# Performance work log

Hardware: AMD Instinct MI355X
Metric: run time of the kernel (lower is better)

## Reference

```python
import jax, jax.numpy as jnp
import numpy as np

DIM, NH, NS = 384, 8, 3
HID = int(DIM * 4.0)
R1 = max(1, int(min(DIM, HID) * 0.5))   # 192
R2 = max(1, int(min(HID, DIM) * 0.5))   # 192
SPLIT = DIM // NS                        # 128
HD = DIM // NH                           # 48


def _ln(x, g, b, eps=1e-6):
    m = jnp.mean(x, axis=-1, keepdims=True)
    v = jnp.mean(jnp.square(x - m), axis=-1, keepdims=True)
    return (x - m) * jax.lax.rsqrt(v + eps) * g + b


def _dwconv(x, w, b):
    # x: [B, SPLIT, H, W]; w: [SPLIT, 1, 3, 3] depthwise (groups=SPLIT)
    y = jax.lax.conv_general_dilated(
        x, w, window_strides=(1, 1), padding='SAME',
        dimension_numbers=('NCHW', 'OIHW', 'NCHW'),
        feature_group_count=SPLIT)
    return y + b[None, :, None, None]


def setup_inputs() -> dict:
    key = jax.random.key(0)
    ks = jax.random.split(key, 16)
    s = lambda *sh: 0.02
    inp = {
        'x': jax.random.normal(ks[0], (16, DIM, 56, 56), jnp.float32),
        'dw_w0': jax.random.normal(ks[1], (SPLIT, 1, 3, 3), jnp.float32) * 0.1,
        'dw_b0': jnp.zeros((SPLIT,), jnp.float32),
        'dw_w1': jax.random.normal(ks[2], (SPLIT, 1, 3, 3), jnp.float32) * 0.1,
        'dw_b1': jnp.zeros((SPLIT,), jnp.float32),
        'ln1_g': jnp.ones((DIM,), jnp.float32),
        'ln1_b': jnp.zeros((DIM,), jnp.float32),
        'qkv_w': jax.random.normal(ks[3], (DIM, 3 * DIM), jnp.float32) * 0.02,
        'proj_w': jax.random.normal(ks[4], (DIM, DIM), jnp.float32) * 0.02,
        'proj_b': jnp.zeros((DIM,), jnp.float32),
        'ln2_g': jnp.ones((DIM,), jnp.float32),
        'ln2_b': jnp.zeros((DIM,), jnp.float32),
        'mlp1_dw': jax.random.normal(ks[5], (DIM, R1), jnp.float32) * 0.02,
        'mlp1_uw': jax.random.normal(ks[6], (R1, HID), jnp.float32) * 0.02,
        'mlp1_ub': jnp.zeros((HID,), jnp.float32),
        'mlp2_dw': jax.random.normal(ks[7], (HID, R2), jnp.float32) * 0.02,
        'mlp2_uw': jax.random.normal(ks[8], (R2, DIM), jnp.float32) * 0.02,
        'mlp2_ub': jnp.zeros((DIM,), jnp.float32),
    }
    return inp


def reference(x, dw_w0, dw_b0, dw_w1, dw_b1, ln1_g, ln1_b, qkv_w,
              proj_w, proj_b, ln2_g, ln2_b,
              mlp1_dw, mlp1_uw, mlp1_ub, mlp2_dw, mlp2_uw, mlp2_ub):
    B, C, H, W = x.shape
    # multi-scale depthwise residual chain
    s0, s1, s2 = jnp.split(x, NS, axis=1)
    s1 = _dwconv(s1 + s0, dw_w0, dw_b0)
    s2 = _dwconv(s2 + s1, dw_w1, dw_b1)
    x = jnp.concatenate([s0, s1, s2], axis=1)

    N = H * W
    x_flat = jnp.transpose(x.reshape(B, C, N), (0, 2, 1))  # [B, N, C]
    y = _ln(x_flat, ln1_g, ln1_b)
    qkv = (y @ qkv_w).reshape(B, N, 3, NH, HD)
    q = jnp.transpose(qkv[:, :, 0], (0, 2, 3, 1))  # [B, NH, HD, N]
    k = jnp.transpose(qkv[:, :, 1], (0, 2, 3, 1))
    v = jnp.transpose(qkv[:, :, 2], (0, 2, 3, 1))
    # L2 normalize over token dim (XCA)
    q = q / jnp.maximum(jnp.linalg.norm(q, axis=-1, keepdims=True), 1e-12)
    k = k / jnp.maximum(jnp.linalg.norm(k, axis=-1, keepdims=True), 1e-12)
    attn = jnp.einsum('bhdn,bhen->bhde', q, k)  # [B, NH, HD, HD]
    attn = jax.nn.softmax(attn, axis=-1)
    y = jnp.einsum('bhde,bhen->bhdn', attn, v)  # [B, NH, HD, N]
    y = jnp.transpose(y, (0, 3, 1, 2)).reshape(B, N, C)
    y = y @ proj_w + proj_b
    x_flat = x_flat + y

    z = _ln(x_flat, ln2_g, ln2_b)
    h = jax.nn.gelu((z @ mlp1_dw) @ mlp1_uw + mlp1_ub, approximate=False)
    z = (h @ mlp2_dw) @ mlp2_uw + mlp2_ub
    x_flat = x_flat + z
    return jnp.transpose(x_flat, (0, 2, 1)).reshape(B, C, H, W)
```

## Files before the change

kernel.cpp:

```cpp
#include <hip/hip_runtime.h>


typedef __attribute__((ext_vector_type(8))) short short8;
typedef __attribute__((ext_vector_type(4))) float floatx4;

#define NB 16
#define DIM 384
#define NTOK 3136
#define TTOK 50176
#define NH 8
#define HD 48

__device__ __forceinline__ unsigned short f2bf(float f) {
  union { float f; unsigned int u; } v; v.f = f;
  unsigned int u = v.u;
  unsigned int r = (u + 0x7FFFu + ((u >> 16) & 1u)) >> 16;
  return (unsigned short)r;
}
__device__ __forceinline__ float bf2f(unsigned short h) {
  union { unsigned int u; float f; } v; v.u = ((unsigned int)h) << 16;
  return v.f;
}

__device__ __forceinline__ void gload_lds16(const unsigned short* g, unsigned short* l) {
  __builtin_amdgcn_global_load_lds(
      (const __attribute__((address_space(1))) unsigned int*)g,
      (__attribute__((address_space(3))) unsigned int*)l, 16, 0, 0);
}

__global__ void zero_f32(float* __restrict__ p, int n) {
  int g = blockIdx.x * 256 + threadIdx.x;
  if (g < n) p[g] = 0.f;
}

__global__ void wtrans(const float* __restrict__ w, unsigned short* __restrict__ wt,
                       int K, int N) {
  int g = blockIdx.x * 256 + threadIdx.x;
  if (g < K * N) {
    int k = g / N, n = g % N;
    wt[(size_t)n * K + k] = f2bf(w[g]);
  }
}

__global__ void dwconv(const float* __restrict__ a, long bsA,
                       const float* __restrict__ b2, long bsB,
                       const float* __restrict__ w, const float* __restrict__ bias,
                       float* __restrict__ dst) {
  int g = blockIdx.x * 256 + threadIdx.x;
  int xx = g % 56;
  int yy = (g / 56) % 56;
  int c  = (g / NTOK) % 128;
  int b  = g / (NTOK * 128);
  const float* pa = a  + (size_t)b * bsA + (size_t)c * NTOK;
  const float* pb = b2 + (size_t)b * bsB + (size_t)c * NTOK;
  float acc = bias[c];
  #pragma unroll
  for (int ky = 0; ky < 3; ky++) {
    int y2 = yy + ky - 1;
    if (y2 < 0 || y2 >= 56) continue;
    #pragma unroll
    for (int kx = 0; kx < 3; kx++) {
      int x2 = xx + kx - 1;
      if (x2 < 0 || x2 >= 56) continue;
      acc += w[c * 9 + ky * 3 + kx] * (pa[y2 * 56 + x2] + pb[y2 * 56 + x2]);
    }
  }
  dst[((size_t)b * 128 + c) * NTOK + yy * 56 + xx] = acc;
}

__global__ __launch_bounds__(256) void build_ln1(
    const float* __restrict__ x, const float* __restrict__ s1,
    const float* __restrict__ s2, const float* __restrict__ g,
    const float* __restrict__ bb, float* __restrict__ xflat,
    unsigned short* __restrict__ y) {
  int tkn = blockIdx.x * 4 + (threadIdx.x >> 6);
  int lane = threadIdx.x & 63;
  int b = tkn / NTOK, n = tkn % NTOK;
  float v[6];
  float s = 0.f, sq = 0.f;
  #pragma unroll
  for (int i = 0; i < 6; i++) {
    int c = lane + i * 64;
    float t;
    if (c < 128)      t = x[((size_t)b * DIM + c) * NTOK + n];
    else if (c < 256) t = s1[((size_t)b * 128 + (c - 128)) * NTOK + n];
    else              t = s2[((size_t)b * 128 + (c - 256)) * NTOK + n];
    v[i] = t; s += t; sq += t * t;
  }
  #pragma unroll
  for (int off = 32; off; off >>= 1) {
    s += __shfl_xor(s, off);
    sq += __shfl_xor(sq, off);
  }
  float mean = s * (1.f / DIM);
  float var = sq * (1.f / DIM) - mean * mean;
  float rs = rsqrtf(var + 1e-6f);
  #pragma unroll
  for (int i = 0; i < 6; i++) {
    int c = lane + i * 64;
    size_t o = (size_t)tkn * DIM + c;
    xflat[o] = v[i];
    y[o] = f2bf((v[i] - mean) * rs * g[c] + bb[c]);
  }
}

__global__ __launch_bounds__(256) void ln_rows(
    const float* __restrict__ in, const float* __restrict__ g,
    const float* __restrict__ bb, unsigned short* __restrict__ out) {
  int tkn = blockIdx.x * 4 + (threadIdx.x >> 6);
  int lane = threadIdx.x & 63;
  const float* row = in + (size_t)tkn * DIM;
  float v[6];
  float s = 0.f, sq = 0.f;
  #pragma unroll
  for (int i = 0; i < 6; i++) {
    int c = lane + i * 64;
    v[i] = row[c]; s += v[i]; sq += v[i] * v[i];
  }
  #pragma unroll
  for (int off = 32; off; off >>= 1) {
    s += __shfl_xor(s, off);
    sq += __shfl_xor(sq, off);
  }
  float mean = s * (1.f / DIM);
  float var = sq * (1.f / DIM) - mean * mean;
  float rs = rsqrtf(var + 1e-6f);
  #pragma unroll
  for (int i = 0; i < 6; i++) {
    int c = lane + i * 64;
    out[(size_t)tkn * DIM + c] = f2bf((v[i] - mean) * rs * g[c] + bb[c]);
  }
}

template<int BN, int MODE>
__global__ __launch_bounds__(256) void gemm128(
    const unsigned short* __restrict__ A, const unsigned short* __restrict__ Bt,
    const float* __restrict__ bias, const float* __restrict__ resid,
    void* __restrict__ out, int M, int N, int K) {
  constexpr int MT = (BN == 128) ? 4 : 2;
  constexpr int NT = 4;
  __shared__ __align__(16) unsigned short As[128 * 32];
  __shared__ __align__(16) unsigned short Bs[BN * 32];
  const int tid = threadIdx.x;
  const int w = tid >> 6, lane = tid & 63;
  const int quad = lane >> 4, r16 = lane & 15;
  const int row0 = blockIdx.y * 128, col0 = blockIdx.x * BN;
  const int wm = (BN == 128) ? (w >> 1) * 64 : w * 32;
  const int wn = (BN == 128) ? (w & 1) * 64 : 0;
  const int lrow = lane >> 2;
  const int lcol = (lane & 3) * 8;

  const unsigned short* aP0 = A + (size_t)(row0 + w * 32 + lrow) * K + lcol;
  const unsigned short* aP1 = aP0 + (size_t)16 * K;
  const unsigned short* bP0 = Bt + (size_t)(col0 + ((BN == 128) ? w * 32 : w * 16) + lrow) * K + lcol;
  const unsigned short* bP1 = bP0 + (size_t)16 * K;

  floatx4 acc[MT][NT] = {};

  for (int k0 = 0; k0 < K; k0 += 32) {
    gload_lds16(aP0 + k0, &As[(2 * w) * 512]);
    gload_lds16(aP1 + k0, &As[(2 * w + 1) * 512]);
    if (BN == 128) {
      gload_lds16(bP0 + k0, &Bs[(2 * w) * 512]);
      gload_lds16(bP1 + k0, &Bs[(2 * w + 1) * 512]);
    } else {
      gload_lds16(bP0 + k0, &Bs[w * 512]);
    }
    __syncthreads();
    short8 af[MT], bfr[NT];
    #pragma unroll
    for (int mi = 0; mi < MT; mi++)
      af[mi] = *(const short8*)(&As[(wm + mi * 16 + r16) * 32 + quad * 8]);
    #pragma unroll
    for (int ni = 0; ni < NT; ni++)
      bfr[ni] = *(const short8*)(&Bs[(wn + ni * 16 + r16) * 32 + quad * 8]);
    #pragma unroll
    for (int mi = 0; mi < MT; mi++)
      #pragma unroll
      for (int ni = 0; ni < NT; ni++)
        acc[mi][ni] = __builtin_amdgcn_mfma_f32_16x16x32_bf16(af[mi], bfr[ni], acc[mi][ni], 0, 0, 0);
    __syncthreads();
  }

  #pragma unroll
  for (int mi = 0; mi < MT; mi++)
    #pragma unroll
    for (int ni = 0; ni < NT; ni++)
      #pragma unroll
      for (int p = 0; p < 4; p++) {
        int row = row0 + wm + mi * 16 + quad * 4 + p;
        int col = col0 + wn + ni * 16 + r16;
        size_t idx = (size_t)row * N + col;
        float v = acc[mi][ni][p];
        if (MODE == 0) {
          ((unsigned short*)out)[idx] = f2bf(v);
        } else if (MODE == 1) {
          v += bias[col];
          v = 0.5f * v * (1.0f + erff(v * 0.70710678118654752f));
          ((unsigned short*)out)[idx] = f2bf(v);
        } else {
          v += bias[col] + resid[idx];
          ((float*)out)[idx] = v;
        }
      }
}

__global__ __launch_bounds__(256) void attn_partial(
    const unsigned short* __restrict__ qkv, float* __restrict__ S,
    float* __restrict__ sq) {
  __shared__ float qs[64][48];
  __shared__ float ks[64][48];
  int blk = blockIdx.x;
  int b = blk / 392, rem = blk % 392;
  int h = rem / 49, chunk = rem % 49;
  int t = threadIdx.x;
  #pragma unroll
  for (int i = 0; i < 12; i++) {
    int idx = t + i * 256;
    int r = idx / 48, d = idx % 48;
    size_t ro = ((size_t)b * NTOK + chunk * 64 + r) * 1152 + h * HD;
    qs[r][d] = bf2f(qkv[ro + d]);
    ks[r][d] = bf2f(qkv[ro + 384 + d]);
  }
  __syncthreads();
  int d0 = (t >> 4) * 3, e0 = (t & 15) * 3;
  float acc[3][3] = {};
  #pragma unroll 4
  for (int r = 0; r < 64; r++) {
    float q0 = qs[r][d0], q1 = qs[r][d0 + 1], q2 = qs[r][d0 + 2];
    float k0 = ks[r][e0], k1 = ks[r][e0 + 1], k2 = ks[r][e0 + 2];
    acc[0][0] += q0 * k0; acc[0][1] += q0 * k1; acc[0][2] += q0 * k2;
    acc[1][0] += q1 * k0; acc[1][1] += q1 * k1; acc[1][2] += q1 * k2;
    acc[2][0] += q2 * k0; acc[2][1] += q2 * k1; acc[2][2] += q2 * k2;
  }
  float* Sp = S + (size_t)(b * NH + h) * 2304;
  #pragma unroll
  for (int i = 0; i < 3; i++)
    #pragma unroll
    for (int j = 0; j < 3; j++)
      atomicAdd(&Sp[(d0 + i) * 48 + e0 + j], acc[i][j]);
  if (t < 48) {
    float s = 0.f;
    for (int r = 0; r < 64; r++) s += qs[r][t] * qs[r][t];
    atomicAdd(&sq[b * 768 + h * HD + t], s);
  } else if (t >= 64 && t < 112) {
    int e = t - 64;
    float s = 0.f;
    for (int r = 0; r < 64; r++) s += ks[r][e] * ks[r][e];
    atomicAdd(&sq[b * 768 + 384 + h * HD + e], s);
  }
}

__global__ __launch_bounds__(64) void attn_softmax(
    float* __restrict__ S, const float* __restrict__ sq) {
  int bh = blockIdx.x, b = bh >> 3, h = bh & 7;
  int t = threadIdx.x;
  if (t >= 48) return;
  float qn = fmaxf(sqrtf(sq[b * 768 + h * HD + t]), 1e-12f);
  float* Sp = S + (size_t)bh * 2304 + t * 48;
  float row[48];
  float m = -1e30f;
  for (int e = 0; e < 48; e++) {
    float kn = fmaxf(sqrtf(sq[b * 768 + 384 + h * HD + e]), 1e-12f);
    row[e] = Sp[e] / (qn * kn);
    m = fmaxf(m, row[e]);
  }
  float ssum = 0.f;
  for (int e = 0; e < 48; e++) { row[e] = expf(row[e] - m); ssum += row[e]; }
  float inv = 1.f / ssum;
  for (int e = 0; e < 48; e++) Sp[e] = row[e] * inv;
}

__global__ __launch_bounds__(256) void attn_apply(
    const unsigned short* __restrict__ qkv, const float* __restrict__ attnb,
    unsigned short* __restrict__ yat) {
  __shared__ float att[48][48];
  int bh = blockIdx.x / 13, chunk = blockIdx.x % 13;
  int b = bh >> 3, h = bh & 7;
  int t = threadIdx.x;
  #pragma unroll
  for (int i = 0; i < 9; i++) {
    int idx = t + i * 256;
    if (idx < 2304) ((float*)att)[idx] = attnb[(size_t)bh * 2304 + idx];
  }
  __syncthreads();
  int n = chunk * 256 + t;
  if (n < NTOK) {
    float v[48];
    size_t ro = ((size_t)b * NTOK + n) * 1152 + 768 + h * HD;
    #pragma unroll
    for (int e = 0; e < 48; e++) v[e] = bf2f(qkv[ro + e]);
    size_t wo = ((size_t)b * NTOK + n) * DIM + h * HD;
    #pragma unroll 4
    for (int d = 0; d < 48; d++) {
      float s = 0.f;
      #pragma unroll
      for (int e = 0; e < 48; e++) s += att[d][e] * v[e];
      yat[wo + d] = f2bf(s);
    }
  }
}

__global__ __launch_bounds__(256) void transpose_out(const float* __restrict__ in,
                                                     float* __restrict__ out) {
  __shared__ float tile[32][33];
  int b = blockIdx.z, ct = blockIdx.y, nt = blockIdx.x;
  int t = threadIdx.x;
  int cc = t & 31, rr = t >> 5;
  #pragma unroll
  for (int i = 0; i < 4; i++) {
    int nn = rr + i * 8;
    tile[nn][cc] = in[((size_t)b * NTOK + nt * 32 + nn) * DIM + ct * 32 + cc];
  }
  __syncthreads();
  #pragma unroll
  for (int i = 0; i < 4; i++) {
    int c2 = rr + i * 8;
    out[((size_t)b * DIM + ct * 32 + c2) * NTOK + nt * 32 + cc] = tile[cc][c2];
  }
}

extern "C" void kernel_launch(void* const* d_in, const int* in_sizes, int n_in,
                              void* d_out, int out_size, void* d_ws, size_t ws_size,
                              hipStream_t stream) {
  const float* x       = (const float*)d_in[0];
  const float* dw_w0   = (const float*)d_in[1];
  const float* dw_b0   = (const float*)d_in[2];
  const float* dw_w1   = (const float*)d_in[3];
  const float* dw_b1   = (const float*)d_in[4];
  const float* ln1_g   = (const float*)d_in[5];
  const float* ln1_b   = (const float*)d_in[6];
  const float* qkv_w   = (const float*)d_in[7];
  const float* proj_w  = (const float*)d_in[8];
  const float* proj_b  = (const float*)d_in[9];
  const float* ln2_g   = (const float*)d_in[10];
  const float* ln2_b   = (const float*)d_in[11];
  const float* mlp1_dw = (const float*)d_in[12];
  const float* mlp1_uw = (const float*)d_in[13];
  const float* mlp1_ub = (const float*)d_in[14];
  const float* mlp2_dw = (const float*)d_in[15];
  const float* mlp2_uw = (const float*)d_in[16];
  const float* mlp2_ub = (const float*)d_in[17];
  float* out = (float*)d_out;
  char* ws = (char*)d_ws;

  float*          xflat = (float*)(ws + 0);
  unsigned short* qkvb  = (unsigned short*)(ws + 77070336);
  float*          s1ws  = (float*)(ws + 77070336);
  float*          s2ws  = (float*)(ws + 102760448);
  unsigned short* ybf   = (unsigned short*)(ws + 192675840);
  unsigned short* yat   = (unsigned short*)(ws + 192675840);
  float*          xres  = (float*)(ws + 77070336);
  unsigned short* zbf   = (unsigned short*)(ws + 0);
  unsigned short* h1    = (unsigned short*)(ws + 38535168);
  unsigned short* h3    = (unsigned short*)(ws + 57802752);
  unsigned short* h2    = (unsigned short*)(ws + 154140672);
  unsigned short* qkvT  = (unsigned short*)(ws + 231211008);
  unsigned short* projT = (unsigned short*)(ws + 232095744);
  unsigned short* m1dT  = (unsigned short*)(ws + 232390656);
  unsigned short* m1uT  = (unsigned short*)(ws + 232538112);
  unsigned short* m2dT  = (unsigned short*)(ws + 233127936);
  unsigned short* m2uT  = (unsigned short*)(ws + 233717760);
  float*          sqbuf = (float*)(ws + 233865216);
  float*          attnb = (float*)(ws + 233914368);

  zero_f32<<<1200, 256, 0, stream>>>(sqbuf, 307200);

  wtrans<<<1728, 256, 0, stream>>>(qkv_w, qkvT, 384, 1152);
  wtrans<<<576, 256, 0, stream>>>(proj_w, projT, 384, 384);
  wtrans<<<288, 256, 0, stream>>>(mlp1_dw, m1dT, 384, 192);
  wtrans<<<1152, 256, 0, stream>>>(mlp1_uw, m1uT, 192, 1536);
  wtrans<<<1152, 256, 0, stream>>>(mlp2_dw, m2dT, 1536, 192);
  wtrans<<<288, 256, 0, stream>>>(mlp2_uw, m2uT, 192, 384);

  dwconv<<<25088, 256, 0, stream>>>(x + 128 * NTOK, (long)DIM * NTOK,
                                    x, (long)DIM * NTOK, dw_w0, dw_b0, s1ws);
  dwconv<<<25088, 256, 0, stream>>>(x + 256 * NTOK, (long)DIM * NTOK,
                                    s1ws, (long)128 * NTOK, dw_w1, dw_b1, s2ws);

  build_ln1<<<12544, 256, 0, stream>>>(x, s1ws, s2ws, ln1_g, ln1_b, xflat, ybf);

  gemm128<128, 0><<<dim3(9, 392), 256, 0, stream>>>(ybf, qkvT, nullptr, nullptr,
                                                    qkvb, TTOK, 1152, 384);
  attn_partial<<<NB * NH * 49, 256, 0, stream>>>(qkvb, attnb, sqbuf);
  attn_softmax<<<NB * NH, 64, 0, stream>>>(attnb, sqbuf);
  attn_apply<<<NB * NH * 13, 256, 0, stream>>>(qkvb, attnb, yat);

  gemm128<128, 2><<<dim3(3, 392), 256, 0, stream>>>(yat, projT, proj_b, xflat,
                                                    xres, TTOK, 384, 384);
  ln_rows<<<12544, 256, 0, stream>>>(xres, ln2_g, ln2_b, zbf);
  gemm128<64, 0><<<dim3(3, 392), 256, 0, stream>>>(zbf, m1dT, nullptr, nullptr,
                                                   h1, TTOK, 192, 384);
  for (int half = 0; half < 2; half++) {
    const unsigned short* h1p = h1 + (size_t)half * 25088 * 192;
    unsigned short* h3p = h3 + (size_t)half * 25088 * 192;
    gemm128<128, 1><<<dim3(12, 196), 256, 0, stream>>>(h1p, m1uT, mlp1_ub, nullptr,
                                                       h2, 25088, 1536, 192);
    gemm128<64, 0><<<dim3(3, 196), 256, 0, stream>>>(h2, m2dT, nullptr, nullptr,
                                                     h3p, 25088, 192, 1536);
  }
  gemm128<128, 2><<<dim3(3, 392), 256, 0, stream>>>(h3, m2uT, mlp2_ub, xres,
                                                    xres, TTOK, 384, 192);
  transpose_out<<<dim3(98, 12, 16), 256, 0, stream>>>(xres, out);
}
```

Before: 992.2 us.

## Restructure LN1 transpose, attention reduction, and attention apply kernels

Result: faster. 885.8 us (-10.7%).

```diff
diff --git a/kernel.cpp b/kernel.cpp
--- a/kernel.cpp
+++ b/kernel.cpp
@@ -26,11 +26,6 @@
   __builtin_amdgcn_global_load_lds(
       (const __attribute__((address_space(1))) unsigned int*)g,
       (__attribute__((address_space(3))) unsigned int*)l, 16, 0, 0);
-}
-
-__global__ void zero_f32(float* __restrict__ p, int n) {
-  int g = blockIdx.x * 256 + threadIdx.x;
-  if (g < n) p[g] = 0.f;
 }
 
 __global__ void wtrans(const float* __restrict__ w, unsigned short* __restrict__ wt,
@@ -73,34 +68,55 @@
     const float* __restrict__ s2, const float* __restrict__ g,
     const float* __restrict__ bb, float* __restrict__ xflat,
     unsigned short* __restrict__ y) {
-  int tkn = blockIdx.x * 4 + (threadIdx.x >> 6);
-  int lane = threadIdx.x & 63;
-  int b = tkn / NTOK, n = tkn % NTOK;
-  float v[6];
-  float s = 0.f, sq = 0.f;
-  #pragma unroll
-  for (int i = 0; i < 6; i++) {
-    int c = lane + i * 64;
-    float t;
-    if (c < 128)      t = x[((size_t)b * DIM + c) * NTOK + n];
-    else if (c < 256) t = s1[((size_t)b * 128 + (c - 128)) * NTOK + n];
-    else              t = s2[((size_t)b * 128 + (c - 256)) * NTOK + n];
-    v[i] = t; s += t; sq += t * t;
-  }
-  #pragma unroll
-  for (int off = 32; off; off >>= 1) {
-    s += __shfl_xor(s, off);
-    sq += __shfl_xor(sq, off);
-  }
-  float mean = s * (1.f / DIM);
-  float var = sq * (1.f / DIM) - mean * mean;
-  float rs = rsqrtf(var + 1e-6f);
-  #pragma unroll
-  for (int i = 0; i < 6; i++) {
-    int c = lane + i * 64;
-    size_t o = (size_t)tkn * DIM + c;
-    xflat[o] = v[i];
-    y[o] = f2bf((v[i] - mean) * rs * g[c] + bb[c]);
+  __shared__ float tile[384 * 33];
+  __shared__ float psum[8][32], psumsq[8][32];
+  __shared__ float smean[32], srs[32];
+  int blk = blockIdx.x;
+  int b = blk / 98, n0 = (blk % 98) * 32;
+  int t = threadIdx.x;
+  int nl = t & 31, crow = t >> 5;
+
+  #pragma unroll 4
+  for (int i = 0; i < 48; i++) {
+    int c = i * 8 + crow;
+    float v;
+    if (c < 128)      v = x[((size_t)b * DIM + c) * NTOK + n0 + nl];
+    else if (c < 256) v = s1[((size_t)b * 128 + (c - 128)) * NTOK + n0 + nl];
+    else              v = s2[((size_t)b * 128 + (c - 256)) * NTOK + n0 + nl];
+    tile[c * 33 + nl] = v;
+  }
+  __syncthreads();
+
+  {
+    int seg = t >> 5, tok = t & 31;
+    float s = 0.f, sq = 0.f;
+    #pragma unroll 8
+    for (int cc = 0; cc < 48; cc++) {
+      float v = tile[(seg * 48 + cc) * 33 + tok];
+      s += v; sq += v * v;
+    }
+    psum[seg][tok] = s; psumsq[seg][tok] = sq;
+  }
+  __syncthreads();
+  if (t < 32) {
+    float s = 0.f, sq = 0.f;
+    #pragma unroll
+    for (int seg = 0; seg < 8; seg++) { s += psum[seg][t]; sq += psumsq[seg][t]; }
+    float mean = s * (1.f / DIM);
+    float var = sq * (1.f / DIM) - mean * mean;
+    smean[t] = mean;
+    srs[t] = rsqrtf(var + 1e-6f);
+  }
+  __syncthreads();
+
+  #pragma unroll 4
+  for (int i = 0; i < 48; i++) {
+    int idx = i * 256 + t;
+    int tok = idx / 384, c = idx - tok * 384;
+    float v = tile[c * 33 + tok];
+    size_t o = (size_t)(b * NTOK + n0 + tok) * DIM + c;
+    xflat[o] = v;
+    y[o] = f2bf((v - smean[tok]) * srs[tok] * g[c] + bb[c]);
   }
 }
 
@@ -206,99 +222,156 @@
 }
 
 __global__ __launch_bounds__(256) void attn_partial(
-    const unsigned short* __restrict__ qkv, float* __restrict__ S,
-    float* __restrict__ sq) {
-  __shared__ float qs[64][48];
-  __shared__ float ks[64][48];
+    const unsigned short* __restrict__ qkv, float* __restrict__ S_part,
+    float* __restrict__ sq_part) {
+  __shared__ float qs[48 * 68];
+  __shared__ float ks[48 * 68];
   int blk = blockIdx.x;
-  int b = blk / 392, rem = blk % 392;
-  int h = rem / 49, chunk = rem % 49;
+  int b = blk / 56, rem = blk % 56;
+  int h = rem / 7, chunk = rem % 7;
   int t = threadIdx.x;
-  #pragma unroll
-  for (int i = 0; i < 12; i++) {
-    int idx = t + i * 256;
-    int r = idx / 48, d = idx % 48;
-    size_t ro = ((size_t)b * NTOK + chunk * 64 + r) * 1152 + h * HD;
-    qs[r][d] = bf2f(qkv[ro + d]);
-    ks[r][d] = bf2f(qkv[ro + 384 + d]);
-  }
-  __syncthreads();
   int d0 = (t >> 4) * 3, e0 = (t & 15) * 3;
-  float acc[3][3] = {};
-  #pragma unroll 4
-  for (int r = 0; r < 64; r++) {
-    float q0 = qs[r][d0], q1 = qs[r][d0 + 1], q2 = qs[r][d0 + 2];
-    float k0 = ks[r][e0], k1 = ks[r][e0 + 1], k2 = ks[r][e0 + 2];
-    acc[0][0] += q0 * k0; acc[0][1] += q0 * k1; acc[0][2] += q0 * k2;
-    acc[1][0] += q1 * k0; acc[1][1] += q1 * k1; acc[1][2] += q1 * k2;
-    acc[2][0] += q2 * k0; acc[2][1] += q2 * k1; acc[2][2] += q2 * k2;
-  }
-  float* Sp = S + (size_t)(b * NH + h) * 2304;
+
+  floatx4 acc4[3][3] = {};
+  floatx4 sqq4 = {}, sqk4 = {};
+
+  for (int tile = 0; tile < 7; tile++) {
+    __syncthreads();
+    int tb = chunk * 448 + tile * 64;
+    #pragma unroll
+    for (int i = 0; i < 12; i++) {
+      int idx = t + i * 256;
+      int r = idx / 48, d = idx - r * 48;
+      size_t ro = ((size_t)b * NTOK + tb + r) * 1152 + h * HD;
+      qs[d * 68 + r] = bf2f(qkv[ro + d]);
+      ks[d * 68 + r] = bf2f(qkv[ro + 384 + d]);
+    }
+    __syncthreads();
+    #pragma unroll 4
+    for (int r4 = 0; r4 < 16; r4++) {
+      floatx4 q4[3], k4[3];
+      #pragma unroll
+      for (int j = 0; j < 3; j++) {
+        q4[j] = *(const floatx4*)(&qs[(d0 + j) * 68 + r4 * 4]);
+        k4[j] = *(const floatx4*)(&ks[(e0 + j) * 68 + r4 * 4]);
+      }
+      #pragma unroll
+      for (int i = 0; i < 3; i++)
+        #pragma unroll
+        for (int j = 0; j < 3; j++)
+          acc4[i][j] += q4[i] * k4[j];
+    }
+    if (t < 48) {
+      #pragma unroll 4
+      for (int r4 = 0; r4 < 16; r4++) {
+        floatx4 v = *(const floatx4*)(&qs[t * 68 + r4 * 4]);
+        sqq4 += v * v;
+      }
+    } else if (t >= 64 && t < 112) {
+      int e = t - 64;
+      #pragma unroll 4
+      for (int r4 = 0; r4 < 16; r4++) {
+        floatx4 v = *(const floatx4*)(&ks[e * 68 + r4 * 4]);
+        sqk4 += v * v;
+      }
+    }
+  }
+
+  int bh = b * NH + h;
+  float* Sp = S_part + ((size_t)chunk * 128 + bh) * 2304;
   #pragma unroll
   for (int i = 0; i < 3; i++)
     #pragma unroll
     for (int j = 0; j < 3; j++)
-      atomicAdd(&Sp[(d0 + i) * 48 + e0 + j], acc[i][j]);
+      Sp[(d0 + i) * 48 + e0 + j] = acc4[i][j][0] + acc4[i][j][1] + acc4[i][j][2] + acc4[i][j][3];
+  if (t < 48)
+    sq_part[(size_t)chunk * 12288 + b * 768 + h * HD + t] = sqq4[0] + sqq4[1] + sqq4[2] + sqq4[3];
+  else if (t >= 64 && t < 112)
+    sq_part[(size_t)chunk * 12288 + b * 768 + 384 + h * HD + (t - 64)] = sqk4[0] + sqk4[1] + sqk4[2] + sqk4[3];
+}
+
+__global__ __launch_bounds__(256) void attn_finish(
+    const float* __restrict__ S_part, const float* __restrict__ sq_part,
+    float* __restrict__ attnb) {
+  __shared__ float qn[48], kn[48];
+  __shared__ float Ss[48 * 49];
+  int bh = blockIdx.x, b = bh >> 3, h = bh & 7;
+  int t = threadIdx.x;
   if (t < 48) {
     float s = 0.f;
-    for (int r = 0; r < 64; r++) s += qs[r][t] * qs[r][t];
-    atomicAdd(&sq[b * 768 + h * HD + t], s);
+    #pragma unroll
+    for (int p = 0; p < 7; p++) s += sq_part[(size_t)p * 12288 + b * 768 + h * HD + t];
+    qn[t] = fmaxf(sqrtf(s), 1e-12f);
   } else if (t >= 64 && t < 112) {
     int e = t - 64;
     float s = 0.f;
-    for (int r = 0; r < 64; r++) s += ks[r][e] * ks[r][e];
-    atomicAdd(&sq[b * 768 + 384 + h * HD + e], s);
-  }
-}
-
-__global__ __launch_bounds__(64) void attn_softmax(
-    float* __restrict__ S, const float* __restrict__ sq) {
-  int bh = blockIdx.x, b = bh >> 3, h = bh & 7;
-  int t = threadIdx.x;
-  if (t >= 48) return;
-  float qn = fmaxf(sqrtf(sq[b * 768 + h * HD + t]), 1e-12f);
-  float* Sp = S + (size_t)bh * 2304 + t * 48;
-  float row[48];
-  float m = -1e30f;
-  for (int e = 0; e < 48; e++) {
-    float kn = fmaxf(sqrtf(sq[b * 768 + 384 + h * HD + e]), 1e-12f);
-    row[e] = Sp[e] / (qn * kn);
-    m = fmaxf(m, row[e]);
-  }
-  float ssum = 0.f;
-  for (int e = 0; e < 48; e++) { row[e] = expf(row[e] - m); ssum += row[e]; }
-  float inv = 1.f / ssum;
-  for (int e = 0; e < 48; e++) Sp[e] = row[e] * inv;
+    #pragma unroll
+    for (int p = 0; p < 7; p++) s += sq_part[(size_t)p * 12288 + b * 768 + 384 + h * HD + e];
+    kn[e] = fmaxf(sqrtf(s), 1e-12f);
+  }
+  __syncthreads();
+  #pragma unroll
+  for (int j = 0; j < 9; j++) {
+    int idx = j * 256 + t;
+    float s = 0.f;
+    #pragma unroll
+    for (int p = 0; p < 7; p++) s += S_part[((size_t)p * 128 + bh) * 2304 + idx];
+    int d = idx / 48, e = idx - d * 48;
+    Ss[d * 49 + e] = s / (qn[d] * kn[e]);
+  }
+  __syncthreads();
+  if (t < 48) {
+    float m = -1e30f;
+    for (int e = 0; e < 48; e++) m = fmaxf(m, Ss[t * 49 + e]);
+    float ssum = 0.f;
+    float ex[48];
+    for (int e = 0; e < 48; e++) { ex[e] = expf(Ss[t * 49 + e] - m); ssum += ex[e]; }
+    float inv = 1.f / ssum;
+    float* op = attnb + (size_t)bh * 2304 + t * 48;
+    for (int e = 0; e < 48; e++) op[e] = ex[e] * inv;
+  }
 }
 
 __global__ __launch_bounds__(256) void attn_apply(
     const unsigned short* __restrict__ qkv, const float* __restrict__ attnb,
     unsigned short* __restrict__ yat) {
-  __shared__ float att[48][48];
-  int bh = blockIdx.x / 13, chunk = blockIdx.x % 13;
+  __shared__ float at[48 * 52];
+  __shared__ float vs[64 * 56];
+  int bh = blockIdx.x / 49, chunk = blockIdx.x % 49;
   int b = bh >> 3, h = bh & 7;
   int t = threadIdx.x;
+  int lane = t & 63, w = t >> 6;
   #pragma unroll
   for (int i = 0; i < 9; i++) {
     int idx = t + i * 256;
-    if (idx < 2304) ((float*)att)[idx] = attnb[(size_t)bh * 2304 + idx];
-  }
-  __syncthreads();
-  int n = chunk * 256 + t;
-  if (n < NTOK) {
-    float v[48];
-    size_t ro = ((size_t)b * NTOK + n) * 1152 + 768 + h * HD;
-    #pragma unroll
-    for (int e = 0; e < 48; e++) v[e] = bf2f(qkv[ro + e]);
-    size_t wo = ((size_t)b * NTOK + n) * DIM + h * HD;
-    #pragma unroll 4
-    for (int d = 0; d < 48; d++) {
-      float s = 0.f;
-      #pragma unroll
-      for (int e = 0; e < 48; e++) s += att[d][e] * v[e];
-      yat[wo + d] = f2bf(s);
-    }
-  }
+    if (idx < 2304) at[(idx / 48) * 52 + idx % 48] = attnb[(size_t)bh * 2304 + idx];
+  }
+  #pragma unroll
+  for (int i = 0; i < 12; i++) {
+    int idx = t + i * 256;
+    int r = idx / 48, d = idx - r * 48;
+    vs[r * 56 + d] = bf2f(qkv[((size_t)b * NTOK + chunk * 64 + r) * 1152 + 768 + h * HD + d]);
+  }
+  __syncthreads();
+  floatx4 v4[12];
+  #pragma unroll
+  for (int j = 0; j < 12; j++)
+    v4[j] = *(const floatx4*)(&vs[lane * 56 + j * 4]);
+  float r[12];
+  #pragma unroll
+  for (int dd = 0; dd < 12; dd++) {
+    int d = w * 12 + dd;
+    floatx4 a = {};
+    #pragma unroll
+    for (int j = 0; j < 12; j++)
+      a += *(const floatx4*)(&at[d * 52 + j * 4]) * v4[j];
+    r[dd] = a[0] + a[1] + a[2] + a[3];
+  }
+  size_t wo = ((size_t)b * NTOK + chunk * 64 + lane) * DIM + h * HD + w * 12;
+  unsigned int* op = (unsigned int*)(yat + wo);
+  #pragma unroll
+  for (int j = 0; j < 6; j++)
+    op[j] = (unsigned int)f2bf(r[2 * j]) | ((unsigned int)f2bf(r[2 * j + 1]) << 16);
 }
 
 __global__ __launch_bounds__(256) void transpose_out(const float* __restrict__ in,
@@ -349,6 +422,8 @@
   float*          s1ws  = (float*)(ws + 77070336);
   float*          s2ws  = (float*)(ws + 102760448);
   unsigned short* ybf   = (unsigned short*)(ws + 192675840);
+  float*          S_part  = (float*)(ws + 192675840);
+  float*          sq_part = (float*)(ws + 200933376);
   unsigned short* yat   = (unsigned short*)(ws + 192675840);
   float*          xres  = (float*)(ws + 77070336);
   unsigned short* zbf   = (unsigned short*)(ws + 0);
@@ -361,10 +436,7 @@
   unsigned short* m1uT  = (unsigned short*)(ws + 232538112);
   unsigned short* m2dT  = (unsigned short*)(ws + 233127936);
   unsigned short* m2uT  = (unsigned short*)(ws + 233717760);
-  float*          sqbuf = (float*)(ws + 233865216);
   float*          attnb = (float*)(ws + 233914368);
-
-  zero_f32<<<1200, 256, 0, stream>>>(sqbuf, 307200);
 
   wtrans<<<1728, 256, 0, stream>>>(qkv_w, qkvT, 384, 1152);
   wtrans<<<576, 256, 0, stream>>>(proj_w, projT, 384, 384);
@@ -378,13 +450,13 @@
   dwconv<<<25088, 256, 0, stream>>>(x + 256 * NTOK, (long)DIM * NTOK,
                                     s1ws, (long)128 * NTOK, dw_w1, dw_b1, s2ws);
 
-  build_ln1<<<12544, 256, 0, stream>>>(x, s1ws, s2ws, ln1_g, ln1_b, xflat, ybf);
+  build_ln1<<<1568, 256, 0, stream>>>(x, s1ws, s2ws, ln1_g, ln1_b, xflat, ybf);
 
   gemm128<128, 0><<<dim3(9, 392), 256, 0, stream>>>(ybf, qkvT, nullptr, nullptr,
                                                     qkvb, TTOK, 1152, 384);
-  attn_partial<<<NB * NH * 49, 256, 0, stream>>>(qkvb, attnb, sqbuf);
-  attn_softmax<<<NB * NH, 64, 0, stream>>>(attnb, sqbuf);
-  attn_apply<<<NB * NH * 13, 256, 0, stream>>>(qkvb, attnb, yat);
+  attn_partial<<<NB * NH * 7, 256, 0, stream>>>(qkvb, S_part, sq_part);
+  attn_finish<<<NB * NH, 256, 0, stream>>>(S_part, sq_part, attnb);
+  attn_apply<<<NB * NH * 49, 256, 0, stream>>>(qkvb, attnb, yat);
 
   gemm128<128, 2><<<dim3(3, 392), 256, 0, stream>>>(yat, projT, proj_b, xflat,
                                                     xres, TTOK, 384, 384);
```
